# Optimization experiments

Hardware: AMD Instinct MI355X
Metric: run time of the kernel (lower is better)

The kernel has to match this reference:

```python
import jax, jax.numpy as jnp
import numpy as np
from jax import lax

B, L, V, E, H = 256, 512, 256, 256, 1024


def setup_inputs() -> dict:
    key = jax.random.key(0)
    k1, k2, k3, k4, k5 = jax.random.split(key, 5)
    x = jax.random.randint(k1, (B, L), 0, V, dtype=jnp.int64)
    hidden = jnp.zeros((B, H), dtype=jnp.float32)
    emb_table = jax.random.normal(k2, (V, E), dtype=jnp.float32)  # nn.Embedding default init ~N(0,1)
    W_e = 0.01 * jax.random.normal(k3, (E, H), dtype=jnp.float32)
    W_h = 0.01 * jax.random.normal(k4, (H, H), dtype=jnp.float32)
    W_o = 0.01 * jax.random.normal(k5, (H, V), dtype=jnp.float32)
    return {"x": x, "hidden": hidden, "emb_table": emb_table, "W_e": W_e, "W_h": W_h, "W_o": W_o}


def reference(x, hidden, emb_table, W_e, W_h, W_o):
    # Precompute input projection for all timesteps in one batched GEMM:
    # emb_table[x] : [B, L, E];  x_proj : [L, B, H] (time-major for scan)
    x_proj = jnp.einsum('ble,eh->lbh', emb_table[x], W_e)

    def step(h_prev, x_t):
        h_t = jnp.tanh(x_t + h_prev @ W_h)  # [B, H]
        return h_t, h_t

    final_hidden, outs = lax.scan(step, hidden, x_proj)  # outs: [L, B, H]
    # logits: [B, L, V]
    logits = jnp.einsum('lbh,hv->blv', outs, W_o)
    return logits, final_hidden
```

## Files before the change

kernel.cpp:

```cpp
#include <hip/hip_runtime.h>
#include <hip/hip_bf16.h>
#include <math.h>

#define B_ 256
#define L_ 512
#define V_ 256
#define E_ 256
#define H_ 1024

typedef float  f32x4  __attribute__((ext_vector_type(4)));
typedef short  bf16x8 __attribute__((ext_vector_type(8)));
typedef unsigned int u32;
typedef unsigned char u8;

static __device__ __forceinline__ ushort f2bf(float v) {
    __hip_bfloat16 b = __float2bfloat16(v);
    return *reinterpret_cast<ushort*>(&b);
}

static __device__ __forceinline__ float ftanh(float z) {
    float e = __expf(2.f * z);
    return 1.f - 2.f / (e + 1.f);
}

__global__ void k_transpose_bf16(const float* __restrict__ in, ushort* __restrict__ out,
                                 int R, int C) {
    __shared__ float tile[64][65];
    int bx = blockIdx.x, by = blockIdx.y;
    int tid = threadIdx.x;
    int g = tid >> 6, l = tid & 63;
    for (int i = 0; i < 16; ++i) {
        int r = g * 16 + i;
        tile[r][l] = in[(size_t)(by * 64 + r) * C + bx * 64 + l];
    }
    __syncthreads();
    for (int i = 0; i < 16; ++i) {
        int c = g * 16 + i;
        out[(size_t)(bx * 64 + c) * R + by * 64 + l] = f2bf(tile[l][c]);
    }
}

__global__ void k_zero(u32* __restrict__ p, int n) {
    int i = blockIdx.x * blockDim.x + threadIdx.x;
    if (i < n) p[i] = 0u;
}

__global__ void k_pack_h0(const float* __restrict__ hid, ushort* __restrict__ ringA,
                          ushort* __restrict__ ringB) {
    int i = blockIdx.x * blockDim.x + threadIdx.x;
    ushort v = f2bf(hid[i]);
    int half = i >> 17;
    int off = i & 131071;
    if (half == 0) ringA[off] = v; else ringB[off] = v;
}

__global__ void k_proj(const float* __restrict__ emb, const float* __restrict__ We,
                       float* __restrict__ proj) {
    __shared__ float er[E_];
    int t = blockIdx.x;
    int h = blockIdx.y * 256 + threadIdx.x;
    er[threadIdx.x] = emb[t * E_ + threadIdx.x];
    __syncthreads();
    float acc = 0.f;
#pragma unroll 8
    for (int e = 0; e < E_; ++e) acc += er[e] * We[(size_t)e * H_ + h];
    proj[(size_t)t * H_ + h] = acc;
}

__global__ __launch_bounds__(256, 1) void k_scan(
    const int* __restrict__ xs, const float* __restrict__ proj,
    const ushort* __restrict__ WhT, const ushort* __restrict__ WoT,
    ushort* __restrict__ ringA, ushort* __restrict__ ringB,
    float* __restrict__ logits, float* __restrict__ final_h,
    u8* __restrict__ flags)
{
    __shared__ ushort lds_w[32 * 1024];
    __shared__ ushort panel[16 * 1024];
    __shared__ float  red[2][16][17];
    __shared__ ushort stile[16 * 32];

    int tid = threadIdx.x;
    int w = tid >> 6, lane = tid & 63;
    int l15 = lane & 15, l4 = lane >> 4;
    int bid = blockIdx.x;
    int rg = bid & 7, cg = bid >> 3;
    int c0 = cg * 32;

    {
        const char* wsrc = (const char*)(WhT + (size_t)c0 * H_);
        char* wd = (char*)lds_w;
        for (int i = 0; i < 16; ++i) {
            int chunk = (w * 16 + i) * 1024;
            int o = chunk + lane * 16;
            int row = o >> 11, b = o & 2047;
            int so = row * 2048 + (b ^ ((row & 7) << 4));
            __builtin_amdgcn_global_load_lds(
                (const __attribute__((address_space(1))) void*)(wsrc + so),
                (__attribute__((address_space(3))) void*)(wd + chunk), 16, 0, 0);
        }
    }

    int as = (l15 & 7) << 4;
    const char* wa = (const char*)lds_w + (size_t)((w & 1) * 16 + l15) * 2048;
    int vcol0 = (cg & 15) * 16;
    const ushort* wo = WoT + (size_t)(vcol0 + l15) * H_;

    for (int p = 0; p <= 2 * L_ + 2; ++p) {
        int hx = p & 1, s = p >> 1;
        int px = (p - 1) & 1, ps = (p - 1) >> 1;
        bool doStage = (p <= 2 * L_ + 1);
        bool doPoll = doStage && (s >= 1);

        ushort* ringR = hx ? ringB : ringA;

        if (w == 0 && doPoll) {
            const u8* fp = flags + ((size_t)(hx * 8 + rg) * 513 + s) * 32 + lane;
            u32 v = 1u;
            while (true) {
                if (lane < 32)
                    asm volatile("global_load_ubyte %0, %1, off sc0 sc1\n\t"
                                 "s_waitcnt vmcnt(0)" : "=v"(v) : "v"(fp) : "memory");
                if (__ballot(v != 0u) == ~0ull) break;
            }
        }
        __syncthreads();

        f32x4 tv[8];
        if (doStage) {
            const char* hsrc = (const char*)(ringR + (size_t)(s & 1) * 128 * H_
                                             + (size_t)(rg * 16) * H_) + tid * 16;
#pragma unroll
            for (int i = 0; i < 8; ++i)
                asm volatile("global_load_dwordx4 %0, %1, off sc0 sc1"
                             : "=v"(tv[i]) : "v"(hsrc + i * 4096) : "memory");
        }

        if (p >= 1) {
            if (w == 0 && ps < L_) {
                ushort* ringW = px ? ringB : ringA;
                int r = lane >> 2, seg = lane & 3;
                f32x4 d = *(const f32x4*)&stile[r * 32 + seg * 8];
                char* dst = (char*)(ringW + (size_t)((ps + 1) & 1) * 128 * H_
                                    + (size_t)(rg * 16 + r) * H_ + c0 + seg * 8);
                asm volatile("global_store_dwordx4 %0, %1, off sc0 sc1"
                             :: "v"(dst), "v"(d) : "memory");
                asm volatile("s_waitcnt vmcnt(0)" ::: "memory");
                if (lane == 0) {
                    u8* fdst = flags + ((size_t)(px * 8 + rg) * 513 + (ps + 1)) * 32 + cg;
                    u32 one = 1u;
                    asm volatile("global_store_byte %0, %1, off sc0 sc1"
                                 :: "v"(fdst), "v"(one) : "memory");
                }
            }
            if (w == 2 && ps >= 1 && cg < 16) {
                int r = lane >> 2, c4 = (lane & 3) * 4;
                f32x4 o;
#pragma unroll
                for (int j = 0; j < 4; ++j) o[j] = red[0][r][c4 + j] + red[1][r][c4 + j];
                int grow = px * 128 + rg * 16 + r;
                *(f32x4*)&logits[((size_t)grow * L_ + (ps - 1)) * V_ + vcol0 + c4] = o;
            }
        }

        float pv[4];
        if (w < 2 && doStage && s < L_) {
#pragma unroll
            for (int j = 0; j < 4; ++j) {
                int grow = hx * 128 + rg * 16 + l4 * 4 + j;
                pv[j] = proj[(size_t)xs[grow * L_ + s] * H_ + c0 + w * 16 + l15];
            }
        }

        if (doStage) {
            asm volatile("s_waitcnt vmcnt(0)" ::: "memory");
#pragma unroll
            for (int i = 0; i < 8; ++i) {
                int o = i * 4096 + tid * 16;
                int row = o >> 11, b = o & 2047;
                *(f32x4*)((char*)panel + row * 2048 + (b ^ ((row & 7) << 4))) = tv[i];
            }
        }
        __syncthreads();

        if (w < 2 && doStage && s < L_) {
            const char* ha = (const char*)panel + l15 * 2048;
            f32x4 acc0 = {0.f,0.f,0.f,0.f}, acc1 = {0.f,0.f,0.f,0.f};
#pragma unroll
            for (int kk = 0; kk < 32; kk += 2) {
                int kb0 = (kk * 32 + l4 * 8) * 2;
                int kb1 = ((kk + 1) * 32 + l4 * 8) * 2;
                bf16x8 af0 = *(const bf16x8*)(ha + (kb0 ^ as));
                bf16x8 bf0 = *(const bf16x8*)(wa + (kb0 ^ as));
                bf16x8 af1 = *(const bf16x8*)(ha + (kb1 ^ as));
                bf16x8 bf1 = *(const bf16x8*)(wa + (kb1 ^ as));
                acc0 = __builtin_amdgcn_mfma_f32_16x16x32_bf16(af0, bf0, acc0, 0, 0, 0);
                acc1 = __builtin_amdgcn_mfma_f32_16x16x32_bf16(af1, bf1, acc1, 0, 0, 0);
            }
#pragma unroll
            for (int j = 0; j < 4; ++j) {
                int lrow = l4 * 4 + j;
                float hv = ftanh((acc0[j] + acc1[j]) + pv[j]);
                stile[lrow * 32 + w * 16 + l15] = f2bf(hv);
                if (s == L_ - 1) {
                    int grow = hx * 128 + rg * 16 + lrow;
                    final_h[(size_t)grow * H_ + c0 + w * 16 + l15] = hv;
                }
            }
        }

        if (w >= 2 && doStage && s >= 1 && cg < 16) {
            const char* ha = (const char*)panel + l15 * 2048;
            int kh = w - 2;
            f32x4 acc0 = {0.f,0.f,0.f,0.f}, acc1 = {0.f,0.f,0.f,0.f};
#pragma unroll
            for (int kk = 0; kk < 16; kk += 2) {
                int k0 = kh * 512 + kk * 32 + l4 * 8;
                int k1 = k0 + 32;
                bf16x8 a0 = *(const bf16x8*)(ha + ((2 * k0) ^ as));
                bf16x8 b0 = *(const bf16x8*)(wo + k0);
                bf16x8 a1 = *(const bf16x8*)(ha + ((2 * k1) ^ as));
                bf16x8 b1 = *(const bf16x8*)(wo + k1);
                acc0 = __builtin_amdgcn_mfma_f32_16x16x32_bf16(a0, b0, acc0, 0, 0, 0);
                acc1 = __builtin_amdgcn_mfma_f32_16x16x32_bf16(a1, b1, acc1, 0, 0, 0);
            }
#pragma unroll
            for (int j = 0; j < 4; ++j) red[kh][l4 * 4 + j][l15] = acc0[j] + acc1[j];
        }
        __syncthreads();
    }
}

extern "C" void kernel_launch(void* const* d_in, const int* in_sizes, int n_in,
                              void* d_out, int out_size, void* d_ws, size_t ws_size,
                              hipStream_t stream)
{
    const int*   x   = (const int*)d_in[0];
    const float* hid = (const float*)d_in[1];
    const float* emb = (const float*)d_in[2];
    const float* We  = (const float*)d_in[3];
    const float* Wh  = (const float*)d_in[4];
    const float* Wo  = (const float*)d_in[5];

    float* logits  = (float*)d_out;
    float* final_h = logits + (size_t)B_ * L_ * V_;

    char* ws = (char*)d_ws;
    float*  proj  = (float*)(ws);
    ushort* WhT   = (ushort*)(ws + (1u << 20));
    ushort* WoT   = (ushort*)(ws + 3u * (1u << 20));
    ushort* ringA = (ushort*)(ws + 3u * (1u << 20) + (1u << 19));
    ushort* ringB = (ushort*)(ws + 4u * (1u << 20));
    u8*     flags = (u8*)(ws + 4u * (1u << 20) + (1u << 19));

    const int FN = 2 * 8 * 513 * 32 / 4;
    k_zero<<<dim3((FN + 255) / 256), 256, 0, stream>>>((u32*)flags, FN);
    k_transpose_bf16<<<dim3(16, 16), 256, 0, stream>>>(Wh, WhT, H_, H_);
    k_transpose_bf16<<<dim3(4, 16),  256, 0, stream>>>(Wo, WoT, H_, V_);
    k_pack_h0<<<dim3(B_ * H_ / 256), 256, 0, stream>>>(hid, ringA, ringB);
    k_proj<<<dim3(256, 4), 256, 0, stream>>>(emb, We, proj);

    k_scan<<<dim3(256), 256, 0, stream>>>(x, proj, WhT, WoT, ringA, ringB,
                                          logits, final_h, flags);
}
```

Before: 2.461 ms.

## Warp-specialize scan loop with double-buffered panel and one barrier per phase

Restructures the persistent recurrent scan so waves 0-1 compute the recurrent GEMM and tanh from the previous phase's panel while waves 2-3 load the next hidden-state panel and compute the output-projection GEMM. The panel, the reduction buffer and the staging tile are double-buffered, which removes one __syncthreads per phase. Each compute wave now stores its own 16-column slice and raises its own flag, and flags grow from 32 to 64 per row group, letting polling for the next phase overlap with the current compute. This lengthens the pipeline by one phase and uses more LDS, and the cross-block flag protocol becomes more intricate.

```diff
diff --git a/kernel.cpp b/kernel.cpp
--- a/kernel.cpp
+++ b/kernel.cpp
@@ -75,9 +75,9 @@
     u8* __restrict__ flags)
 {
     __shared__ ushort lds_w[32 * 1024];
-    __shared__ ushort panel[16 * 1024];
-    __shared__ float  red[2][16][17];
-    __shared__ ushort stile[16 * 32];
+    __shared__ ushort panel[2][16 * 1024];
+    __shared__ float  red[2][2][16][17];
+    __shared__ ushort stile[2][16][16];
 
     int tid = threadIdx.x;
     int w = tid >> 6, lane = tid & 63;
@@ -85,6 +85,7 @@
     int bid = blockIdx.x;
     int rg = bid & 7, cg = bid >> 3;
     int c0 = cg * 32;
+    int as = (l15 & 7) << 4;
 
     {
         const char* wsrc = (const char*)(WhT + (size_t)c0 * H_);
@@ -99,132 +100,133 @@
                 (__attribute__((address_space(3))) void*)(wd + chunk), 16, 0, 0);
         }
     }
-
-    int as = (l15 & 7) << 4;
+    asm volatile("s_waitcnt vmcnt(0)" ::: "memory");
+    __syncthreads();
+
     const char* wa = (const char*)lds_w + (size_t)((w & 1) * 16 + l15) * 2048;
     int vcol0 = (cg & 15) * 16;
     const ushort* wo = WoT + (size_t)(vcol0 + l15) * H_;
-
-    for (int p = 0; p <= 2 * L_ + 2; ++p) {
+    int sl = tid - 128;
+
+    for (int p = 0; p <= 2 * L_ + 3; ++p) {
         int hx = p & 1, s = p >> 1;
         int px = (p - 1) & 1, ps = (p - 1) >> 1;
+        int qx = (p - 2) & 1, qs = (p - 2) >> 1;
         bool doStage = (p <= 2 * L_ + 1);
-        bool doPoll = doStage && (s >= 1);
-
-        ushort* ringR = hx ? ringB : ringA;
-
-        if (w == 0 && doPoll) {
-            const u8* fp = flags + ((size_t)(hx * 8 + rg) * 513 + s) * 32 + lane;
-            u32 v = 1u;
-            while (true) {
-                if (lane < 32)
-                    asm volatile("global_load_ubyte %0, %1, off sc0 sc1\n\t"
-                                 "s_waitcnt vmcnt(0)" : "=v"(v) : "v"(fp) : "memory");
-                if (__ballot(v != 0u) == ~0ull) break;
-            }
-        }
-        __syncthreads();
-
-        f32x4 tv[8];
-        if (doStage) {
-            const char* hsrc = (const char*)(ringR + (size_t)(s & 1) * 128 * H_
-                                             + (size_t)(rg * 16) * H_) + tid * 16;
-#pragma unroll
-            for (int i = 0; i < 8; ++i)
-                asm volatile("global_load_dwordx4 %0, %1, off sc0 sc1"
-                             : "=v"(tv[i]) : "v"(hsrc + i * 4096) : "memory");
-        }
-
-        if (p >= 1) {
-            if (w == 0 && ps < L_) {
+        bool doA = (p >= 1) && (ps < L_);
+        bool doB = (p >= 1) && (ps >= 1) && (ps <= L_) && (cg < 16);
+        bool doPend = (p >= 2) && (qs >= 1) && (qs <= L_) && (cg < 16);
+
+        if (w < 2) {
+            if (doA) {
+                float pv[4];
+#pragma unroll
+                for (int j = 0; j < 4; ++j) {
+                    int grow = px * 128 + rg * 16 + l4 * 4 + j;
+                    pv[j] = proj[(size_t)xs[grow * L_ + ps] * H_ + c0 + w * 16 + l15];
+                }
+                const char* ha = (const char*)panel[px] + l15 * 2048;
+                f32x4 acc0 = {0.f,0.f,0.f,0.f}, acc1 = {0.f,0.f,0.f,0.f};
+#pragma unroll
+                for (int kk = 0; kk < 32; kk += 2) {
+                    int kb0 = (kk * 32 + l4 * 8) * 2;
+                    int kb1 = ((kk + 1) * 32 + l4 * 8) * 2;
+                    bf16x8 af0 = *(const bf16x8*)(ha + (kb0 ^ as));
+                    bf16x8 bf0 = *(const bf16x8*)(wa + (kb0 ^ as));
+                    bf16x8 af1 = *(const bf16x8*)(ha + (kb1 ^ as));
+                    bf16x8 bf1 = *(const bf16x8*)(wa + (kb1 ^ as));
+                    acc0 = __builtin_amdgcn_mfma_f32_16x16x32_bf16(af0, bf0, acc0, 0, 0, 0);
+                    acc1 = __builtin_amdgcn_mfma_f32_16x16x32_bf16(af1, bf1, acc1, 0, 0, 0);
+                }
+#pragma unroll
+                for (int j = 0; j < 4; ++j) {
+                    int lrow = l4 * 4 + j;
+                    float hv = ftanh((acc0[j] + acc1[j]) + pv[j]);
+                    stile[w][lrow][l15] = f2bf(hv);
+                    if (ps == L_ - 1) {
+                        int grow = px * 128 + rg * 16 + lrow;
+                        final_h[(size_t)grow * H_ + c0 + w * 16 + l15] = hv;
+                    }
+                }
+                asm volatile("s_waitcnt lgkmcnt(0)" ::: "memory");
                 ushort* ringW = px ? ringB : ringA;
-                int r = lane >> 2, seg = lane & 3;
-                f32x4 d = *(const f32x4*)&stile[r * 32 + seg * 8];
-                char* dst = (char*)(ringW + (size_t)((ps + 1) & 1) * 128 * H_
-                                    + (size_t)(rg * 16 + r) * H_ + c0 + seg * 8);
-                asm volatile("global_store_dwordx4 %0, %1, off sc0 sc1"
-                             :: "v"(dst), "v"(d) : "memory");
+                if (lane < 32) {
+                    int row = lane >> 1, half = lane & 1;
+                    f32x4 d = *(const f32x4*)&stile[w][row][half * 8];
+                    char* dst = (char*)(ringW + (size_t)((ps + 1) & 1) * 128 * H_
+                                        + (size_t)(rg * 16 + row) * H_ + c0 + w * 16 + half * 8);
+                    asm volatile("global_store_dwordx4 %0, %1, off sc0 sc1"
+                                 :: "v"(dst), "v"(d) : "memory");
+                }
                 asm volatile("s_waitcnt vmcnt(0)" ::: "memory");
                 if (lane == 0) {
-                    u8* fdst = flags + ((size_t)(px * 8 + rg) * 513 + (ps + 1)) * 32 + cg;
+                    u8* fdst = flags + ((size_t)(px * 8 + rg) * 513 + (ps + 1)) * 64 + cg * 2 + w;
                     u32 one = 1u;
                     asm volatile("global_store_byte %0, %1, off sc0 sc1"
                                  :: "v"(fdst), "v"(one) : "memory");
                 }
             }
-            if (w == 2 && ps >= 1 && cg < 16) {
-                int r = lane >> 2, c4 = (lane & 3) * 4;
+            if (w == 0) {
+                int pn = p + 1;
+                if (pn <= 2 * L_ + 1 && (pn >> 1) >= 1) {
+                    int hxn = pn & 1, sn = pn >> 1;
+                    const u8* fp = flags + ((size_t)(hxn * 8 + rg) * 513 + sn) * 64 + lane;
+                    u32 v;
+                    while (true) {
+                        asm volatile("global_load_ubyte %0, %1, off sc0 sc1\n\t"
+                                     "s_waitcnt vmcnt(0)" : "=v"(v) : "v"(fp) : "memory");
+                        if (__ballot(v != 0u) == ~0ull) break;
+                    }
+                }
+            }
+        } else {
+            f32x4 tv[16];
+            if (doStage) {
+                const ushort* ringR = hx ? ringB : ringA;
+                const char* hsrc = (const char*)(ringR + (size_t)(s & 1) * 128 * H_
+                                                 + (size_t)(rg * 16) * H_) + sl * 16;
+#pragma unroll
+                for (int i = 0; i < 16; ++i)
+                    asm volatile("global_load_dwordx4 %0, %1, off sc0 sc1"
+                                 : "=v"(tv[i]) : "v"(hsrc + i * 2048) : "memory");
+            }
+            if (w == 3 && doPend) {
+                int r = lane >> 2, cq = (lane & 3) * 4;
                 f32x4 o;
 #pragma unroll
-                for (int j = 0; j < 4; ++j) o[j] = red[0][r][c4 + j] + red[1][r][c4 + j];
-                int grow = px * 128 + rg * 16 + r;
-                *(f32x4*)&logits[((size_t)grow * L_ + (ps - 1)) * V_ + vcol0 + c4] = o;
-            }
-        }
-
-        float pv[4];
-        if (w < 2 && doStage && s < L_) {
-#pragma unroll
-            for (int j = 0; j < 4; ++j) {
-                int grow = hx * 128 + rg * 16 + l4 * 4 + j;
-                pv[j] = proj[(size_t)xs[grow * L_ + s] * H_ + c0 + w * 16 + l15];
-            }
-        }
-
-        if (doStage) {
-            asm volatile("s_waitcnt vmcnt(0)" ::: "memory");
-#pragma unroll
-            for (int i = 0; i < 8; ++i) {
-                int o = i * 4096 + tid * 16;
-                int row = o >> 11, b = o & 2047;
-                *(f32x4*)((char*)panel + row * 2048 + (b ^ ((row & 7) << 4))) = tv[i];
-            }
-        }
-        __syncthreads();
-
-        if (w < 2 && doStage && s < L_) {
-            const char* ha = (const char*)panel + l15 * 2048;
-            f32x4 acc0 = {0.f,0.f,0.f,0.f}, acc1 = {0.f,0.f,0.f,0.f};
-#pragma unroll
-            for (int kk = 0; kk < 32; kk += 2) {
-                int kb0 = (kk * 32 + l4 * 8) * 2;
-                int kb1 = ((kk + 1) * 32 + l4 * 8) * 2;
-                bf16x8 af0 = *(const bf16x8*)(ha + (kb0 ^ as));
-                bf16x8 bf0 = *(const bf16x8*)(wa + (kb0 ^ as));
-                bf16x8 af1 = *(const bf16x8*)(ha + (kb1 ^ as));
-                bf16x8 bf1 = *(const bf16x8*)(wa + (kb1 ^ as));
-                acc0 = __builtin_amdgcn_mfma_f32_16x16x32_bf16(af0, bf0, acc0, 0, 0, 0);
-                acc1 = __builtin_amdgcn_mfma_f32_16x16x32_bf16(af1, bf1, acc1, 0, 0, 0);
-            }
-#pragma unroll
-            for (int j = 0; j < 4; ++j) {
-                int lrow = l4 * 4 + j;
-                float hv = ftanh((acc0[j] + acc1[j]) + pv[j]);
-                stile[lrow * 32 + w * 16 + l15] = f2bf(hv);
-                if (s == L_ - 1) {
-                    int grow = hx * 128 + rg * 16 + lrow;
-                    final_h[(size_t)grow * H_ + c0 + w * 16 + l15] = hv;
-                }
-            }
-        }
-
-        if (w >= 2 && doStage && s >= 1 && cg < 16) {
-            const char* ha = (const char*)panel + l15 * 2048;
-            int kh = w - 2;
-            f32x4 acc0 = {0.f,0.f,0.f,0.f}, acc1 = {0.f,0.f,0.f,0.f};
-#pragma unroll
-            for (int kk = 0; kk < 16; kk += 2) {
-                int k0 = kh * 512 + kk * 32 + l4 * 8;
-                int k1 = k0 + 32;
-                bf16x8 a0 = *(const bf16x8*)(ha + ((2 * k0) ^ as));
-                bf16x8 b0 = *(const bf16x8*)(wo + k0);
-                bf16x8 a1 = *(const bf16x8*)(ha + ((2 * k1) ^ as));
-                bf16x8 b1 = *(const bf16x8*)(wo + k1);
-                acc0 = __builtin_amdgcn_mfma_f32_16x16x32_bf16(a0, b0, acc0, 0, 0, 0);
-                acc1 = __builtin_amdgcn_mfma_f32_16x16x32_bf16(a1, b1, acc1, 0, 0, 0);
-            }
-#pragma unroll
-            for (int j = 0; j < 4; ++j) red[kh][l4 * 4 + j][l15] = acc0[j] + acc1[j];
+                for (int j = 0; j < 4; ++j)
+                    o[j] = red[(p - 1) & 1][0][r][cq + j] + red[(p - 1) & 1][1][r][cq + j];
+                int grow = qx * 128 + rg * 16 + r;
+                *(f32x4*)&logits[((size_t)grow * L_ + (qs - 1)) * V_ + vcol0 + cq] = o;
+            }
+            if (doB) {
+                const char* ha = (const char*)panel[px] + l15 * 2048;
+                int kh = w - 2;
+                f32x4 acc0 = {0.f,0.f,0.f,0.f}, acc1 = {0.f,0.f,0.f,0.f};
+#pragma unroll
+                for (int kk = 0; kk < 16; kk += 2) {
+                    int k0 = kh * 512 + kk * 32 + l4 * 8;
+                    int k1 = k0 + 32;
+                    bf16x8 a0 = *(const bf16x8*)(ha + ((2 * k0) ^ as));
+                    bf16x8 b0 = *(const bf16x8*)(wo + k0);
+                    bf16x8 a1 = *(const bf16x8*)(ha + ((2 * k1) ^ as));
+                    bf16x8 b1 = *(const bf16x8*)(wo + k1);
+                    acc0 = __builtin_amdgcn_mfma_f32_16x16x32_bf16(a0, b0, acc0, 0, 0, 0);
+                    acc1 = __builtin_amdgcn_mfma_f32_16x16x32_bf16(a1, b1, acc1, 0, 0, 0);
+                }
+#pragma unroll
+                for (int j = 0; j < 4; ++j)
+                    red[p & 1][kh][l4 * 4 + j][l15] = acc0[j] + acc1[j];
+            }
+            if (doStage) {
+                asm volatile("s_waitcnt vmcnt(0)" ::: "memory");
+                char* hd = (char*)panel[hx];
+#pragma unroll
+                for (int i = 0; i < 16; ++i) {
+                    int b = sl * 16;
+                    *(f32x4*)(hd + i * 2048 + (b ^ ((i & 7) << 4))) = tv[i];
+                }
+            }
         }
         __syncthreads();
     }
@@ -252,7 +254,7 @@
     ushort* ringB = (ushort*)(ws + 4u * (1u << 20));
     u8*     flags = (u8*)(ws + 4u * (1u << 20) + (1u << 19));
 
-    const int FN = 2 * 8 * 513 * 32 / 4;
+    const int FN = 2 * 8 * 513 * 64 / 4;
     k_zero<<<dim3((FN + 255) / 256), 256, 0, stream>>>((u32*)flags, FN);
     k_transpose_bf16<<<dim3(16, 16), 256, 0, stream>>>(Wh, WhT, H_, H_);
     k_transpose_bf16<<<dim3(4, 16),  256, 0, stream>>>(Wo, WoT, H_, V_);
```

Result: slower. 4.784 ms (+94.4%).
